# Kernel tuning notes

Measured on AMD Instinct MI355X. Metric: run time of the kernel, lower is better.

The kernel has to match this reference:

```python
import jax, jax.numpy as jnp
import numpy as np

NUM_HEADS = 16
DIM_HEAD = 64
SCALE = DIM_HEAD ** -0.5
ROPE_BASE = 10000.0


def _rope(t):
    # t: [b, h, n, d] -> rotary embedding with rotate-half convention
    n, d = t.shape[2], t.shape[3]
    inv_freq = 1.0 / (ROPE_BASE ** (jnp.arange(0, d, 2, dtype=jnp.float32) / d))
    freqs = jnp.arange(n, dtype=jnp.float32)[:, None] * inv_freq[None, :]  # [n, d/2]
    cos = jnp.concatenate([jnp.cos(freqs), jnp.cos(freqs)], axis=-1)  # [n, d]
    sin = jnp.concatenate([jnp.sin(freqs), jnp.sin(freqs)], axis=-1)
    t1, t2 = jnp.split(t, 2, axis=-1)
    rot = jnp.concatenate([-t2, t1], axis=-1)
    return t * cos + rot * sin


def setup_inputs() -> dict:
    key = jax.random.key(0)
    k1, k2, k3 = jax.random.split(key, 3)
    B, N, D = 2, 2049, 1024  # 2048 patches + 1 cls token
    x = jax.random.normal(k1, (B, N, D), dtype=jnp.float32)
    ln_gamma = jnp.ones((D,), dtype=jnp.float32)
    ln_beta = jnp.zeros((D,), dtype=jnp.float32)
    w_qkv = jax.random.normal(k2, (D, 3 * NUM_HEADS * DIM_HEAD), dtype=jnp.float32) * 0.02
    w_out = jax.random.normal(k3, (NUM_HEADS * DIM_HEAD, D), dtype=jnp.float32) * 0.02
    return {"x": x, "ln_gamma": ln_gamma, "ln_beta": ln_beta, "w_qkv": w_qkv, "w_out": w_out}


def reference(x, ln_gamma, ln_beta, w_qkv, w_out):
    B, N, D = x.shape
    # LayerNorm (eps=1e-5, torch default)
    mu = jnp.mean(x, axis=-1, keepdims=True)
    var = jnp.mean(jnp.square(x - mu), axis=-1, keepdims=True)
    xn = (x - mu) * jax.lax.rsqrt(var + 1e-5) * ln_gamma + ln_beta
    # QKV projection (no bias)
    qkv = xn @ w_qkv  # [B, N, 3*H*Dh]
    q, k, v = jnp.split(qkv, 3, axis=-1)
    def to_heads(t):
        return t.reshape(B, N, NUM_HEADS, DIM_HEAD).transpose(0, 2, 1, 3)  # [B,H,N,Dh]
    q, k, v = to_heads(q), to_heads(k), to_heads(v)
    # cls token excluded from RoPE
    q = jnp.concatenate([q[:, :, :1, :], _rope(q[:, :, 1:, :])], axis=2)
    k = jnp.concatenate([k[:, :, :1, :], _rope(k[:, :, 1:, :])], axis=2)
    dots = jnp.einsum('bhqd,bhkd->bhqk', q, k) * SCALE
    attn = jax.nn.softmax(dots, axis=-1)
    out = jnp.einsum('bhqk,bhkd->bhqd', attn, v)
    out = out.transpose(0, 2, 1, 3).reshape(B, N, NUM_HEADS * DIM_HEAD)
    return out @ w_out
```

## Files before the change

kernel.cpp:

```cpp
#include <hip/hip_runtime.h>

#define B_    2
#define N_    2049
#define NPAD  2112
#define D_    1024
#define H_    16
#define DH    64
#define MROWS (B_ * N_)
#define MPAD  4224
#define QSCALE 0.18033688011117674f

using bf16x8 = __attribute__((ext_vector_type(8))) short;
using f32x4  = __attribute__((ext_vector_type(4))) float;
using f32x16 = __attribute__((ext_vector_type(16))) float;

#define AS1 __attribute__((address_space(1)))
#define AS3 __attribute__((address_space(3)))

__device__ __forceinline__ float bf2f(short s) {
  union { unsigned u; float f; } a; a.u = ((unsigned)(unsigned short)s) << 16; return a.f;
}
__device__ __forceinline__ short f2bf(float f) {
  union { float f; unsigned u; } a; a.f = f;
  unsigned r = a.u + 0x7fffu + ((a.u >> 16) & 1u);
  return (short)(r >> 16);
}
__device__ __forceinline__ unsigned pack_trunc(float lo, float hi) {
  union { float f; unsigned u; } a, b; a.f = lo; b.f = hi;
  return (b.u & 0xffff0000u) | (a.u >> 16);
}
__device__ __forceinline__ float hexp2(float x) { return __builtin_amdgcn_exp2f(x); }
__device__ __forceinline__ void dma16(const short* g, AS3 short* l) {
  __builtin_amdgcn_global_load_lds((const AS1 unsigned*)g, (AS3 unsigned*)l, 16, 0, 0);
}

__device__ __forceinline__ size_t tiled_off(int m, int k) {
  return ((size_t)(m >> 7) << 17)
       + (size_t)(((k >> 5) << 12)
       + ((((m & 127) >> 4)) << 9)
       + (((((m & 15) << 2) | ((k & 31) >> 3))) << 3)
       + (k & 7));
}

__global__ __launch_bounds__(256) void prep_kernel(const float* __restrict__ x,
                                                   const float* __restrict__ gamma,
                                                   const float* __restrict__ beta,
                                                   short* __restrict__ xn,
                                                   const float* __restrict__ w_qkv,
                                                   short* __restrict__ wqkvT,
                                                   const float* __restrict__ w_out,
                                                   short* __restrict__ woutT) {
  int blk = blockIdx.x;
  int tid = threadIdx.x;
  __shared__ float T[64][65];
  __shared__ float sb[4], s2b[4];

  if (blk < MROWS) {
    int row = blk;
    const float4 v = ((const float4*)(x + (size_t)row * D_))[tid];
    float s  = v.x + v.y + v.z + v.w;
    float ss = v.x * v.x + v.y * v.y + v.z * v.z + v.w * v.w;
    for (int o = 1; o < 64; o <<= 1) { s += __shfl_xor(s, o, 64); ss += __shfl_xor(ss, o, 64); }
    int wid = tid >> 6;
    if ((tid & 63) == 0) { sb[wid] = s; s2b[wid] = ss; }
    __syncthreads();
    float st  = sb[0] + sb[1] + sb[2] + sb[3];
    float sst = s2b[0] + s2b[1] + s2b[2] + s2b[3];
    float mu  = st * (1.0f / D_);
    float var = sst * (1.0f / D_) - mu * mu;
    float rs  = rsqrtf(var + 1e-5f);
    const float4 g  = ((const float4*)gamma)[tid];
    const float4 be = ((const float4*)beta)[tid];
    short4 o4;
    o4.x = f2bf((v.x - mu) * rs * g.x + be.x);
    o4.y = f2bf((v.y - mu) * rs * g.y + be.y);
    o4.z = f2bf((v.z - mu) * rs * g.z + be.z);
    o4.w = f2bf((v.w - mu) * rs * g.w + be.w);
    *(short4*)(xn + tiled_off(row, tid * 4)) = o4;
    return;
  }

  const float* in; short* out; int Nn, t2;
  int b2 = blk - MROWS;
  if (b2 < 768) { in = w_qkv; out = wqkvT; Nn = 3072; t2 = b2; }
  else          { in = w_out; out = woutT; Nn = 1024; t2 = b2 - 768; }
  int k0 = (t2 & 15) * 64;
  int n0 = (t2 >> 4) * 64;
  int r = tid >> 2, c0 = (tid & 3) * 16;
  const float* ip = in + (size_t)(k0 + r) * Nn + n0 + c0;
  #pragma unroll
  for (int j = 0; j < 4; ++j) {
    float4 v = *(const float4*)(ip + j * 4);
    T[r][c0 + j * 4 + 0] = v.x; T[r][c0 + j * 4 + 1] = v.y;
    T[r][c0 + j * 4 + 2] = v.z; T[r][c0 + j * 4 + 3] = v.w;
  }
  __syncthreads();
  bf16x8 w0, w1;
  #pragma unroll
  for (int j = 0; j < 8; ++j) {
    w0[j] = f2bf(T[c0 + j][r]);
    w1[j] = f2bf(T[c0 + 8 + j][r]);
  }
  *(bf16x8*)(out + tiled_off(n0 + r, k0 + c0))     = w0;
  *(bf16x8*)(out + tiled_off(n0 + r, k0 + c0 + 8)) = w1;
}

#define BM 128
#define BK 32
template <typename OutT>
__global__ __launch_bounds__(256) void gemm128(const short* __restrict__ A,
                                               const short* __restrict__ BT,
                                               OutT* __restrict__ C,
                                               int Mstore, int Ncols, int K) {
  int lane = threadIdx.x & 63, wid = threadIdx.x >> 6;
  int quad = lane >> 4, l16 = lane & 15;
  int wr = wid >> 1, wc = wid & 1;
  int chunk = gridDim.x >> 3;
  int swz = (blockIdx.x & 7) * chunk + (blockIdx.x >> 3);
  int mb = swz % 33, nb = swz / 33;
  int m0 = mb * BM;
  int n0 = nb * BM;

  __shared__ __align__(16) short Abuf[2][BM * BK];
  __shared__ __align__(16) short Bbuf[2][BM * BK];
  AS3 short* AbufL = (AS3 short*)&Abuf[0][0];
  AS3 short* BbufL = (AS3 short*)&Bbuf[0][0];

  f32x4 acc[4][4] = {};

  const short* Ap = A  + ((size_t)(m0 >> 7) << 17);
  const short* Bp = BT + ((size_t)(n0 >> 7) << 17);

  auto stage = [&](int kt, int bb) {
    #pragma unroll
    for (int i = 0; i < 2; ++i) {
      int j = wid * 2 + i;
      dma16(Ap + ((size_t)kt << 12) + j * 512 + lane * 8, AbufL + bb * (BM * BK) + j * 512);
      dma16(Bp + ((size_t)kt << 12) + j * 512 + lane * 8, BbufL + bb * (BM * BK) + j * 512);
    }
  };

  stage(0, 0);
  __syncthreads();

  int KT = K / BK;
  for (int kt = 0; kt < KT; ++kt) {
    int cur = kt & 1;
    if (kt + 1 < KT) stage(kt + 1, cur ^ 1);
    const short* Ab = &Abuf[cur][0];
    const short* Bb = &Bbuf[cur][0];
    bf16x8 af[4], bfr[4];
    #pragma unroll
    for (int s = 0; s < 4; ++s)
      af[s] = *(const bf16x8*)&Ab[(wr * 64 + s * 16 + l16) * BK + quad * 8];
    #pragma unroll
    for (int t = 0; t < 4; ++t)
      bfr[t] = *(const bf16x8*)&Bb[(wc * 64 + t * 16 + l16) * BK + quad * 8];
    #pragma unroll
    for (int s = 0; s < 4; ++s)
      #pragma unroll
      for (int t = 0; t < 4; ++t)
        acc[s][t] = __builtin_amdgcn_mfma_f32_16x16x32_bf16(af[s], bfr[t], acc[s][t], 0, 0, 0);
    __syncthreads();
  }

  #pragma unroll
  for (int s = 0; s < 4; ++s)
    #pragma unroll
    for (int r = 0; r < 4; ++r) {
      int row = m0 + wr * 64 + s * 16 + quad * 4 + r;
      if (row < Mstore) {
        size_t rb = (size_t)row * Ncols + n0 + wc * 64;
        #pragma unroll
        for (int t = 0; t < 4; ++t) {
          float val = acc[s][t][r];
          if constexpr (sizeof(OutT) == 2)
            C[rb + t * 16 + l16] = (OutT)(unsigned short)f2bf(val);
          else
            C[rb + t * 16 + l16] = (OutT)val;
        }
      }
    }
}

__global__ __launch_bounds__(256) void rope_kernel(const short* __restrict__ qkv,
                                                   short* __restrict__ qg,
                                                   short* __restrict__ kfrag,
                                                   short* __restrict__ vfrag) {
  int bh = blockIdx.y;
  int n0 = blockIdx.x * 64;
  int b = bh >> 4, h = bh & 15;
  int t = threadIdx.x;
  int nl = t >> 2;
  int p  = t & 3;
  int n  = n0 + nl;
  size_t hb = (size_t)bh * NPAD * DH;
  size_t ob = hb + (size_t)n * DH;

  __shared__ short Vt[64][66];
  __shared__ short Kt[64][66];

  bf16x8 oq1 = {}, oq2 = {}, ok1 = {}, ok2 = {};
  short v1s[8] = {}, v2s[8] = {};
  if (n < N_) {
    size_t ib = ((size_t)(b * N_ + n)) * 3072 + h * DH;
    bf16x8 q1v = *(const bf16x8*)(qkv + ib + p * 8);
    bf16x8 q2v = *(const bf16x8*)(qkv + ib + 32 + p * 8);
    bf16x8 k1v = *(const bf16x8*)(qkv + ib + 1024 + p * 8);
    bf16x8 k2v = *(const bf16x8*)(qkv + ib + 1024 + 32 + p * 8);
    bf16x8 v1v = *(const bf16x8*)(qkv + ib + 2048 + p * 8);
    bf16x8 v2v = *(const bf16x8*)(qkv + ib + 2048 + 32 + p * 8);
    #pragma unroll
    for (int j = 0; j < 8; ++j) {
      int i = p * 8 + j;
      float q1 = bf2f(q1v[j]), q2 = bf2f(q2v[j]);
      float k1 = bf2f(k1v[j]), k2 = bf2f(k2v[j]);
      if (n > 0) {
        float ang = (float)(n - 1) * hexp2((float)i * -0.4152410118609203f);
        float rev = ang * 0.15915494309189535f;
        rev = rev - floorf(rev);
        float sn = __builtin_amdgcn_sinf(rev);
        float cs = __builtin_amdgcn_cosf(rev);
        float nq1 = q1 * cs - q2 * sn, nq2 = q2 * cs + q1 * sn;
        float nk1 = k1 * cs - k2 * sn, nk2 = k2 * cs + k1 * sn;
        q1 = nq1; q2 = nq2; k1 = nk1; k2 = nk2;
      }
      oq1[j] = f2bf(q1 * QSCALE); oq2[j] = f2bf(q2 * QSCALE);
      ok1[j] = f2bf(k1); ok2[j] = f2bf(k2);
      v1s[j] = v1v[j]; v2s[j] = v2v[j];
    }
  }
  *(bf16x8*)(qg + ob + p * 8)      = oq1;
  *(bf16x8*)(qg + ob + 32 + p * 8) = oq2;
  #pragma unroll
  for (int j = 0; j < 8; ++j) {
    Vt[nl][p * 8 + j]      = v1s[j];
    Vt[nl][32 + p * 8 + j] = v2s[j];
    Kt[nl][p * 8 + j]      = ok1[j];
    Kt[nl][32 + p * 8 + j] = ok2[j];
  }
  __syncthreads();

  int l = t & 63, c = t >> 6;
  int lk = l & 31, hi = l >> 5;
  size_t tb = hb + (size_t)(n0 >> 6) * 4096;
  bf16x8 wv0, wv1, wk0, wk1;
  #pragma unroll
  for (int i = 0; i < 8; ++i) {
    int keyr = c * 16 + hi * 8 + i;
    wv0[i] = Vt[keyr][lk];
    wv1[i] = Vt[keyr][32 + lk];
    wk0[i] = Kt[lk][keyr];
    wk1[i] = Kt[32 + lk][keyr];
  }
  *(bf16x8*)(vfrag + tb + (size_t)(0 * 4 + c) * 512 + l * 8) = wv0;
  *(bf16x8*)(vfrag + tb + (size_t)(4 + c) * 512 + l * 8)     = wv1;
  *(bf16x8*)(kfrag + tb + (size_t)(0 * 4 + c) * 512 + l * 8) = wk0;
  *(bf16x8*)(kfrag + tb + (size_t)(4 + c) * 512 + l * 8)     = wk1;
}

__global__ __launch_bounds__(256, 3) void attn_kernel(const short* __restrict__ qg,
                                                      const short* __restrict__ kfrag,
                                                      const short* __restrict__ vfrag,
                                                      short* __restrict__ Opart,
                                                      float* __restrict__ lpart) {
  int blk = blockIdx.x;
  int xcd = blk & 7;
  int t_  = blk >> 3;
  int bh  = xcd * 4 + (t_ & 3);
  int u   = t_ >> 2;
  int ks  = (u >= 17) ? 1 : 0;
  int qblk = u - ks * 17;
  int kt0 = ks * 17, kt1 = ks ? 32 : 16;

  int lane = threadIdx.x & 63, wid = threadIdx.x >> 6;
  int q    = lane & 31;
  int half = lane >> 5;
  int q0   = qblk * 128 + wid * 32;
  size_t hb = (size_t)bh * NPAD * DH;
  const short* kf_hb = kfrag + hb;
  const short* vf_hb = vfrag + hb;

  __shared__ __align__(16) short Kbuf[3][4096];
  __shared__ __align__(16) short Vbuf[3][4096];
  AS3 short* KbufL = (AS3 short*)&Kbuf[0][0];
  AS3 short* VbufL = (AS3 short*)&Vbuf[0][0];
  const short* KbufR = &Kbuf[0][0];
  const short* VbufR = &Vbuf[0][0];

  int qr = q0 + q; if (qr >= NPAD) qr = 0;
  const short* qp = qg + hb + (size_t)qr * DH + half * 8;
  bf16x8 qf[4];
  #pragma unroll
  for (int s = 0; s < 4; ++s) qf[s] = *(const bf16x8*)(qp + s * 16);

  f32x16 o0 = {}, o1 = {};
  float lrun = 0.0f;

  auto stage = [&](int kt, int bb) {
    const short* ksrc = kf_hb + (size_t)kt * 4096;
    const short* vsrc = vf_hb + (size_t)kt * 4096;
    #pragma unroll
    for (int i = 0; i < 2; ++i) {
      int j = wid * 2 + i;
      dma16(ksrc + j * 512 + lane * 8, KbufL + bb * 4096 + j * 512);
      dma16(vsrc + j * 512 + lane * 8, VbufL + bb * 4096 + j * 512);
    }
  };

  stage(kt0, 0);
  stage(kt0 + 1, 1);

  for (int kt = kt0; kt <= kt1; ++kt) {
    int rb = (kt - kt0) % 3;
    int k0 = kt * 64;

    asm volatile("s_waitcnt vmcnt(4)" ::: "memory");
    __builtin_amdgcn_s_barrier();

    if (kt + 2 <= kt1) stage(kt + 2, (kt - kt0 + 2) % 3);
    __builtin_amdgcn_sched_barrier(0);

    const short* Vc = VbufR + rb * 4096;
    bf16x8 vf0[4], vf1[4];
    #pragma unroll
    for (int s = 0; s < 4; ++s) {
      vf0[s] = *(const bf16x8*)&Vc[(0 * 4 + s) * 512 + lane * 8];
      vf1[s] = *(const bf16x8*)&Vc[(4 + s) * 512 + lane * 8];
    }

    const short* Kc = KbufR + rb * 4096;
    f32x16 sA = {}, sB = {};
    __builtin_amdgcn_s_setprio(1);
    #pragma unroll
    for (int s = 0; s < 4; ++s) {
      bf16x8 kf0 = *(const bf16x8*)&Kc[(0 * 4 + s) * 512 + lane * 8];
      bf16x8 kf1 = *(const bf16x8*)&Kc[(1 * 4 + s) * 512 + lane * 8];
      sA = __builtin_amdgcn_mfma_f32_32x32x16_bf16(kf0, qf[s], sA, 0, 0, 0);
      sB = __builtin_amdgcn_mfma_f32_32x32x16_bf16(kf1, qf[s], sB, 0, 0, 0);
    }
    __builtin_amdgcn_s_setprio(0);

    if (k0 + 64 > N_) {
      #pragma unroll
      for (int rr = 0; rr < 16; ++rr) {
        int key = (rr & 3) + 8 * (rr >> 2) + 4 * half;
        if (k0 + key >= N_)      sA[rr] = -1e30f;
        if (k0 + 32 + key >= N_) sB[rr] = -1e30f;
      }
    }

    float vsum = 0.0f;
    #pragma unroll
    for (int rr = 0; rr < 16; ++rr) {
      sA[rr] = hexp2(sA[rr]); vsum += sA[rr];
      sB[rr] = hexp2(sB[rr]); vsum += sB[rr];
    }
    lrun += vsum;

    unsigned w[4][4];
    #pragma unroll
    for (int g = 0; g < 2; ++g) {
      #pragma unroll
      for (int fs = 0; fs < 2; ++fs) {
        int b0 = fs * 8;
        float e0, e1, e2, e3, e4, e5, e6, e7;
        if (g == 0) {
          e0 = sA[b0+0]; e1 = sA[b0+1]; e2 = sA[b0+2]; e3 = sA[b0+3];
          e4 = sA[b0+4]; e5 = sA[b0+5]; e6 = sA[b0+6]; e7 = sA[b0+7];
        } else {
          e0 = sB[b0+0]; e1 = sB[b0+1]; e2 = sB[b0+2]; e3 = sB[b0+3];
          e4 = sB[b0+4]; e5 = sB[b0+5]; e6 = sB[b0+6]; e7 = sB[b0+7];
        }
        unsigned X1 = pack_trunc(e0, e1);
        unsigned X2 = pack_trunc(e2, e3);
        unsigned Y1 = pack_trunc(e4, e5);
        unsigned Y2 = pack_trunc(e6, e7);
        asm("v_permlane32_swap_b32 %0, %1" : "+v"(X1), "+v"(Y1));
        asm("v_permlane32_swap_b32 %0, %1" : "+v"(X2), "+v"(Y2));
        int kst = g * 2 + fs;
        w[kst][0] = X1; w[kst][1] = X2; w[kst][2] = Y1; w[kst][3] = Y2;
      }
    }

    __builtin_amdgcn_s_setprio(1);
    #pragma unroll
    for (int kst = 0; kst < 4; ++kst) {
      union { unsigned u[4]; bf16x8 v; } bw;
      bw.u[0] = w[kst][0]; bw.u[1] = w[kst][1]; bw.u[2] = w[kst][2]; bw.u[3] = w[kst][3];
      o0 = __builtin_amdgcn_mfma_f32_32x32x16_bf16(vf0[kst], bw.v, o0, 0, 0, 0);
      o1 = __builtin_amdgcn_mfma_f32_32x32x16_bf16(vf1[kst], bw.v, o1, 0, 0, 0);
    }
    __builtin_amdgcn_s_setprio(0);
  }

  lrun += __shfl_xor(lrun, 32, 64);

  int qrow = q0 + q;
  if (qrow < N_) {
    size_t ob = (((size_t)ks * 32 + bh) * NPAD + qrow) * 64;
    #pragma unroll
    for (int m = 0; m < 2; ++m) {
      #pragma unroll
      for (int gq = 0; gq < 4; ++gq) {
        float a0 = m ? o1[gq*4+0] : o0[gq*4+0];
        float a1 = m ? o1[gq*4+1] : o0[gq*4+1];
        float a2 = m ? o1[gq*4+2] : o0[gq*4+2];
        float a3 = m ? o1[gq*4+3] : o0[gq*4+3];
        short4 st;
        st.x = f2bf(a0); st.y = f2bf(a1); st.z = f2bf(a2); st.w = f2bf(a3);
        int dh = m * 32 + gq * 8 + half * 4;
        *(short4*)(Opart + ob + dh) = st;
      }
    }
    if (half == 0) lpart[((size_t)ks * 32 + bh) * NPAD + qrow] = lrun;
  }
}

__global__ __launch_bounds__(256) void combine_kernel(const short* __restrict__ Opart,
                                                      const float* __restrict__ lpart,
                                                      short* __restrict__ attn_out) {
  int idx = blockIdx.x * 256 + threadIdx.x;
  const int total = 32 * N_ * 16;
  if (idx >= total) return;
  int c4 = idx & 15;
  int t = idx >> 4;
  int n = t % N_;
  int bh = t / N_;
  int b = bh >> 4, h = bh & 15;
  const size_t halfO = (size_t)32 * NPAD * 64;
  size_t off = ((size_t)bh * NPAD + n) * 64 + c4 * 4;
  short4 a  = *(const short4*)(Opart + off);
  short4 bb = *(const short4*)(Opart + halfO + off);
  float la = lpart[(size_t)bh * NPAD + n];
  float lb = lpart[(size_t)32 * NPAD + (size_t)bh * NPAD + n];
  float inv = 1.0f / (la + lb);
  short4 st;
  st.x = f2bf((bf2f(a.x) + bf2f(bb.x)) * inv);
  st.y = f2bf((bf2f(a.y) + bf2f(bb.y)) * inv);
  st.z = f2bf((bf2f(a.z) + bf2f(bb.z)) * inv);
  st.w = f2bf((bf2f(a.w) + bf2f(bb.w)) * inv);
  *(short4*)(attn_out + tiled_off(b * N_ + n, h * DH + c4 * 4)) = st;
}

extern "C" void kernel_launch(void* const* d_in, const int* in_sizes, int n_in,
                              void* d_out, int out_size, void* d_ws, size_t ws_size,
                              hipStream_t stream) {
  const float* x     = (const float*)d_in[0];
  const float* gamma = (const float*)d_in[1];
  const float* beta  = (const float*)d_in[2];
  const float* w_qkv = (const float*)d_in[3];
  const float* w_out = (const float*)d_in[4];

  short* wqkvT = (short*)d_ws;
  short* woutT = wqkvT + (size_t)3072 * 1024;
  short* xn    = woutT + (size_t)1024 * 1024;
  short* qkv   = xn    + (size_t)MPAD * 1024;
  short* qg    = qkv   + (size_t)MPAD * 3072;
  short* kfragG = qg    + (size_t)B_ * H_ * NPAD * DH;
  short* vfragG = kfragG + (size_t)B_ * H_ * NPAD * DH;
  short* attn_out = xn;
  short* Opart = qkv;
  float* lpart = (float*)(qkv + (size_t)2 * 32 * NPAD * 64);

  prep_kernel<<<MROWS + 768 + 256, 256, 0, stream>>>(x, gamma, beta, xn,
                                                     w_qkv, wqkvT, w_out, woutT);
  gemm128<unsigned short><<<792, 256, 0, stream>>>(xn, wqkvT, (unsigned short*)qkv, MROWS, 3072, 1024);
  {
    dim3 g(33, 32);
    rope_kernel<<<g, 256, 0, stream>>>(qkv, qg, kfragG, vfragG);
  }
  attn_kernel<<<8 * 4 * 17 * 2, 256, 0, stream>>>(qg, kfragG, vfragG, Opart, lpart);
  combine_kernel<<<(32 * N_ * 16 + 255) / 256, 256, 0, stream>>>(Opart, lpart, attn_out);
  gemm128<float><<<264, 256, 0, stream>>>(attn_out, woutT, (float*)d_out, MROWS, 1024, 1024);
}
```

Before: 225.6 us.

## Drop split-K attention and combine kernel; normalize output directly in attention

Attention blocks now cover all 33 key tiles instead of splitting keys in two. Each block normalizes its own output and writes it straight into the tiled layout the output GEMM expects, so the combine kernel and the partial O/l buffers are gone. Probability packing also switches from manual truncation to the hardware v_cvt_pk_bf16_f32 instruction. The grid halves from 1088 to 544 blocks, which removes a launch and the partial-buffer traffic but lowers parallelism and lengthens each block's serial loop.

```diff
diff --git a/kernel.cpp b/kernel.cpp
--- a/kernel.cpp
+++ b/kernel.cpp
@@ -24,10 +24,6 @@
   union { float f; unsigned u; } a; a.f = f;
   unsigned r = a.u + 0x7fffu + ((a.u >> 16) & 1u);
   return (short)(r >> 16);
-}
-__device__ __forceinline__ unsigned pack_trunc(float lo, float hi) {
-  union { float f; unsigned u; } a, b; a.f = lo; b.f = hi;
-  return (b.u & 0xffff0000u) | (a.u >> 16);
 }
 __device__ __forceinline__ float hexp2(float x) { return __builtin_amdgcn_exp2f(x); }
 __device__ __forceinline__ void dma16(const short* g, AS3 short* l) {
@@ -262,16 +258,13 @@
 __global__ __launch_bounds__(256, 3) void attn_kernel(const short* __restrict__ qg,
                                                       const short* __restrict__ kfrag,
                                                       const short* __restrict__ vfrag,
-                                                      short* __restrict__ Opart,
-                                                      float* __restrict__ lpart) {
+                                                      short* __restrict__ out) {
   int blk = blockIdx.x;
   int xcd = blk & 7;
   int t_  = blk >> 3;
   int bh  = xcd * 4 + (t_ & 3);
-  int u   = t_ >> 2;
-  int ks  = (u >= 17) ? 1 : 0;
-  int qblk = u - ks * 17;
-  int kt0 = ks * 17, kt1 = ks ? 32 : 16;
+  int qblk = t_ >> 2;
+  int b = bh >> 4, h = bh & 15;
 
   int lane = threadIdx.x & 63, wid = threadIdx.x >> 6;
   int q    = lane & 31;
@@ -308,17 +301,19 @@
     }
   };
 
-  stage(kt0, 0);
-  stage(kt0 + 1, 1);
-
-  for (int kt = kt0; kt <= kt1; ++kt) {
-    int rb = (kt - kt0) % 3;
+  stage(0, 0);
+  stage(1, 1);
+
+  #define NKT 33
+  for (int kt = 0; kt < NKT; ++kt) {
+    int rb = kt % 3;
     int k0 = kt * 64;
 
-    asm volatile("s_waitcnt vmcnt(4)" ::: "memory");
+    if (kt == NKT - 1) asm volatile("s_waitcnt vmcnt(0)" ::: "memory");
+    else               asm volatile("s_waitcnt vmcnt(4)" ::: "memory");
     __builtin_amdgcn_s_barrier();
 
-    if (kt + 2 <= kt1) stage(kt + 2, (kt - kt0 + 2) % 3);
+    if (kt + 2 < NKT) stage(kt + 2, (kt + 2) % 3);
     __builtin_amdgcn_sched_barrier(0);
 
     const short* Vc = VbufR + rb * 4096;
@@ -372,10 +367,11 @@
           e0 = sB[b0+0]; e1 = sB[b0+1]; e2 = sB[b0+2]; e3 = sB[b0+3];
           e4 = sB[b0+4]; e5 = sB[b0+5]; e6 = sB[b0+6]; e7 = sB[b0+7];
         }
-        unsigned X1 = pack_trunc(e0, e1);
-        unsigned X2 = pack_trunc(e2, e3);
-        unsigned Y1 = pack_trunc(e4, e5);
-        unsigned Y2 = pack_trunc(e6, e7);
+        unsigned X1, X2, Y1, Y2;
+        asm("v_cvt_pk_bf16_f32 %0, %1, %2" : "=v"(X1) : "v"(e0), "v"(e1));
+        asm("v_cvt_pk_bf16_f32 %0, %1, %2" : "=v"(X2) : "v"(e2), "v"(e3));
+        asm("v_cvt_pk_bf16_f32 %0, %1, %2" : "=v"(Y1) : "v"(e4), "v"(e5));
+        asm("v_cvt_pk_bf16_f32 %0, %1, %2" : "=v"(Y2) : "v"(e6), "v"(e7));
         asm("v_permlane32_swap_b32 %0, %1" : "+v"(X1), "+v"(Y1));
         asm("v_permlane32_swap_b32 %0, %1" : "+v"(X2), "+v"(Y2));
         int kst = g * 2 + fs;
@@ -398,49 +394,23 @@
 
   int qrow = q0 + q;
   if (qrow < N_) {
-    size_t ob = (((size_t)ks * 32 + bh) * NPAD + qrow) * 64;
+    float inv = 1.0f / lrun;
+    int grow = b * N_ + qrow;
     #pragma unroll
     for (int m = 0; m < 2; ++m) {
       #pragma unroll
       for (int gq = 0; gq < 4; ++gq) {
-        float a0 = m ? o1[gq*4+0] : o0[gq*4+0];
-        float a1 = m ? o1[gq*4+1] : o0[gq*4+1];
-        float a2 = m ? o1[gq*4+2] : o0[gq*4+2];
-        float a3 = m ? o1[gq*4+3] : o0[gq*4+3];
+        float a0 = (m ? o1[gq*4+0] : o0[gq*4+0]) * inv;
+        float a1 = (m ? o1[gq*4+1] : o0[gq*4+1]) * inv;
+        float a2 = (m ? o1[gq*4+2] : o0[gq*4+2]) * inv;
+        float a3 = (m ? o1[gq*4+3] : o0[gq*4+3]) * inv;
         short4 st;
         st.x = f2bf(a0); st.y = f2bf(a1); st.z = f2bf(a2); st.w = f2bf(a3);
         int dh = m * 32 + gq * 8 + half * 4;
-        *(short4*)(Opart + ob + dh) = st;
+        *(short4*)(out + tiled_off(grow, h * DH + dh)) = st;
       }
     }
-    if (half == 0) lpart[((size_t)ks * 32 + bh) * NPAD + qrow] = lrun;
-  }
-}
-
-__global__ __launch_bounds__(256) void combine_kernel(const short* __restrict__ Opart,
-                                                      const float* __restrict__ lpart,
-                                                      short* __restrict__ attn_out) {
-  int idx = blockIdx.x * 256 + threadIdx.x;
-  const int total = 32 * N_ * 16;
-  if (idx >= total) return;
-  int c4 = idx & 15;
-  int t = idx >> 4;
-  int n = t % N_;
-  int bh = t / N_;
-  int b = bh >> 4, h = bh & 15;
-  const size_t halfO = (size_t)32 * NPAD * 64;
-  size_t off = ((size_t)bh * NPAD + n) * 64 + c4 * 4;
-  short4 a  = *(const short4*)(Opart + off);
-  short4 bb = *(const short4*)(Opart + halfO + off);
-  float la = lpart[(size_t)bh * NPAD + n];
-  float lb = lpart[(size_t)32 * NPAD + (size_t)bh * NPAD + n];
-  float inv = 1.0f / (la + lb);
-  short4 st;
-  st.x = f2bf((bf2f(a.x) + bf2f(bb.x)) * inv);
-  st.y = f2bf((bf2f(a.y) + bf2f(bb.y)) * inv);
-  st.z = f2bf((bf2f(a.z) + bf2f(bb.z)) * inv);
-  st.w = f2bf((bf2f(a.w) + bf2f(bb.w)) * inv);
-  *(short4*)(attn_out + tiled_off(b * N_ + n, h * DH + c4 * 4)) = st;
+  }
 }
 
 extern "C" void kernel_launch(void* const* d_in, const int* in_sizes, int n_in,
@@ -460,8 +430,6 @@
   short* kfragG = qg    + (size_t)B_ * H_ * NPAD * DH;
   short* vfragG = kfragG + (size_t)B_ * H_ * NPAD * DH;
   short* attn_out = xn;
-  short* Opart = qkv;
-  float* lpart = (float*)(qkv + (size_t)2 * 32 * NPAD * 64);
 
   prep_kernel<<<MROWS + 768 + 256, 256, 0, stream>>>(x, gamma, beta, xn,
                                                      w_qkv, wqkvT, w_out, woutT);
@@ -470,7 +438,6 @@
     dim3 g(33, 32);
     rope_kernel<<<g, 256, 0, stream>>>(qkv, qg, kfragG, vfragG);
   }
-  attn_kernel<<<8 * 4 * 17 * 2, 256, 0, stream>>>(qg, kfragG, vfragG, Opart, lpart);
-  combine_kernel<<<(32 * N_ * 16 + 255) / 256, 256, 0, stream>>>(Opart, lpart, attn_out);
+  attn_kernel<<<544, 256, 0, stream>>>(qg, kfragG, vfragG, attn_out);
   gemm128<float><<<264, 256, 0, stream>>>(attn_out, woutT, (float*)d_out, MROWS, 1024, 1024);
 }
```

After: 220.9 us. 2.1% less time.
